# Optimization experiments

Hardware: AMD Instinct MI355X
Metric: run time of the kernel (lower is better)

Reference implementation:

```python
import jax, jax.numpy as jnp
import numpy as np

B, T, C = 2, 2048, 1024
H, D = 16, 64
EPS = 1e-6


def _layernorm(x, gamma, beta):
    # Faithful to the torch module: uses unbiased std (Bessel) and divides by (std + eps).
    mean = x.mean(-1, keepdims=True)
    std = jnp.sqrt(jnp.sum((x - mean) ** 2, axis=-1, keepdims=True) / (x.shape[-1] - 1))
    return gamma * (x - mean) / (std + EPS) + beta


def setup_inputs() -> dict:
    key = jax.random.key(0)
    ks = jax.random.split(key, 9)
    s = lambda fan_in: 1.0 / np.sqrt(fan_in)
    return {
        "x": jax.random.normal(ks[0], (B, T, C), dtype=jnp.float32),
        "qkv_w": jax.random.uniform(ks[1], (3 * C, C), jnp.float32, -s(C), s(C)),
        "proj_w": jax.random.uniform(ks[2], (C, C), jnp.float32, -s(C), s(C)),
        "proj_b": jax.random.uniform(ks[3], (C,), jnp.float32, -s(C), s(C)),
        "l1_w": jax.random.uniform(ks[4], (4 * C, C), jnp.float32, -s(C), s(C)),
        "l1_b": jax.random.uniform(ks[5], (4 * C,), jnp.float32, -s(C), s(C)),
        "l3_w": jax.random.uniform(ks[6], (C, 4 * C), jnp.float32, -s(4 * C), s(4 * C)),
        "l3_b": jax.random.uniform(ks[7], (C,), jnp.float32, -s(4 * C), s(4 * C)),
        "ln1_g": jnp.ones((C,), jnp.float32),
        "ln1_b": jnp.zeros((C,), jnp.float32),
        "ln2_g": jnp.ones((C,), jnp.float32),
        "ln2_b": jnp.zeros((C,), jnp.float32),
    }


def _attention(x, qkv_w, proj_w, proj_b):
    Bx, Tx, Cx = x.shape
    qkv = x @ qkv_w.T                      # [B,T,3C]
    q, k, v = jnp.split(qkv, 3, axis=-1)
    q = q.reshape(Bx, Tx, H, D)
    k = k.reshape(Bx, Tx, H, D)
    v = v.reshape(Bx, Tx, H, D)
    scores = jnp.einsum("bthd,bshd->bhts", q, k) * (D ** -0.5)  # [B,H,T,T]
    causal = jnp.tril(jnp.ones((Tx, Tx), dtype=bool))
    scores = jnp.where(causal, scores, -jnp.inf)
    attn = jax.nn.softmax(scores, axis=-1)
    out = jnp.einsum("bhts,bshd->bthd", attn, v).reshape(Bx, Tx, Cx)
    return out @ proj_w.T + proj_b


def _mlp(x, l1_w, l1_b, l3_w, l3_b):
    h = jax.nn.relu(x @ l1_w.T + l1_b)     # [B,T,4C]
    return h @ l3_w.T + l3_b


def reference(x, qkv_w, proj_w, proj_b, l1_w, l1_b, l3_w, l3_b, ln1_g, ln1_b, ln2_g, ln2_b):
    # Dropout is identity in eval mode.
    x1 = x + _attention(_layernorm(x, ln1_g, ln1_b), qkv_w, proj_w, proj_b)
    x2 = x1 + _mlp(_layernorm(x1, ln2_g, ln2_b), l1_w, l1_b, l3_w, l3_b)
    return x2
```

## Files before the change

kernel.cpp:

```cpp
#include <hip/hip_runtime.h>

typedef unsigned short u16;
typedef short short8 __attribute__((ext_vector_type(8)));
typedef float floatx4 __attribute__((ext_vector_type(4)));

#define TT 2048
#define CC 1024

__device__ __forceinline__ u16 f2bf(float f) {
  unsigned int u = __float_as_uint(f);
  u += 0x7fffu + ((u >> 16) & 1u);
  return (u16)(u >> 16);
}

__device__ __forceinline__ unsigned int pk2bf(float a, float b) {
  unsigned int ua = __float_as_uint(a) + 0x8000u;
  unsigned int ub = __float_as_uint(b) + 0x8000u;
  return (ua >> 16) | (ub & 0xffff0000u);
}

__device__ __forceinline__ void glds16(const u16* g, u16* l) {
  __builtin_amdgcn_global_load_lds((const __attribute__((address_space(1))) void*)g,
                                   (__attribute__((address_space(3))) void*)l, 16, 0, 0);
}

__global__ __launch_bounds__(256) void cvt_all_kernel(const float* __restrict__ w0,
                                                      const float* __restrict__ w1,
                                                      const float* __restrict__ w2,
                                                      const float* __restrict__ w3,
                                                      u16* __restrict__ o0,
                                                      u16* __restrict__ o1,
                                                      u16* __restrict__ o2,
                                                      u16* __restrict__ o3) {
  int blk = blockIdx.x;
  const float* in;
  u16* out;
  int base;
  if (blk < 3072)      { in = w0; out = o0; base = 0; }
  else if (blk < 4096) { in = w1; out = o1; base = 3072; }
  else if (blk < 8192) { in = w2; out = o2; base = 4096; }
  else                 { in = w3; out = o3; base = 8192; }
  int i = (blk - base) * 256 + threadIdx.x;
  float4 v = ((const float4*)in)[i];
  ushort4 o;
  o.x = f2bf(v.x); o.y = f2bf(v.y); o.z = f2bf(v.z); o.w = f2bf(v.w);
  ((ushort4*)out)[i] = o;
}

__global__ __launch_bounds__(256) void ln_kernel(const float* __restrict__ x,
                                                 const float* __restrict__ g,
                                                 const float* __restrict__ b,
                                                 u16* __restrict__ out) {
  int row = blockIdx.x;
  int tid = threadIdx.x;
  const float4* xr = (const float4*)(x + (size_t)row * CC);
  float4 v = xr[tid];
  float s = v.x + v.y + v.z + v.w;
  float sq = v.x * v.x + v.y * v.y + v.z * v.z + v.w * v.w;
#pragma unroll
  for (int off = 1; off < 64; off <<= 1) {
    s += __shfl_xor(s, off);
    sq += __shfl_xor(sq, off);
  }
  __shared__ float ss[4], ssq[4];
  int wave = tid >> 6;
  if ((tid & 63) == 0) { ss[wave] = s; ssq[wave] = sq; }
  __syncthreads();
  s = ss[0] + ss[1] + ss[2] + ss[3];
  sq = ssq[0] + ssq[1] + ssq[2] + ssq[3];
  float mean = s * (1.0f / CC);
  float var = (sq - (float)CC * mean * mean) * (1.0f / (CC - 1));
  float inv = 1.0f / (sqrtf(fmaxf(var, 0.0f)) + 1e-6f);
  float4 gv = ((const float4*)g)[tid];
  float4 bv = ((const float4*)b)[tid];
  ushort4 o;
  o.x = f2bf(gv.x * (v.x - mean) * inv + bv.x);
  o.y = f2bf(gv.y * (v.y - mean) * inv + bv.y);
  o.z = f2bf(gv.z * (v.z - mean) * inv + bv.z);
  o.w = f2bf(gv.w * (v.w - mean) * inv + bv.w);
  ((ushort4*)(out + (size_t)row * CC))[tid] = o;
}

template <int BM, int MODE>
__global__ __launch_bounds__(256) void gemm_bt(const u16* __restrict__ A,
                                               const u16* __restrict__ W,
                                               const float* __restrict__ bias,
                                               const float* __restrict__ resid,
                                               float* __restrict__ outf,
                                               u16* __restrict__ outb,
                                               int M, int N, int K, int lda) {
  constexpr int MI = BM / 32;
  __shared__ u16 a_lds[BM * 64];
  __shared__ u16 b_lds[128 * 64];
  int tid = threadIdx.x;
  int w = tid >> 6, lane = tid & 63;
  int l15 = lane & 15, quad = lane >> 4;
  int wm = (w >> 1) * (MI * 16), wn = (w & 1) * 64;
  int tm = blockIdx.x * BM, tn = blockIdx.y * 128;
  size_t koff = (size_t)blockIdx.z * K;
  floatx4 acc[MI][4];
#pragma unroll
  for (int i = 0; i < MI; i++)
#pragma unroll
    for (int j = 0; j < 4; j++) acc[i][j] = (floatx4){0.f, 0.f, 0.f, 0.f};

  int rsub = lane >> 3;
  int cg = (lane & 7) ^ rsub;
  const u16* Ag = A + (size_t)(tm + w * (BM / 4) + rsub) * lda + koff + cg * 8;
  const u16* Bg = W + (size_t)(tn + w * 32 + rsub) * lda + koff + cg * 8;
  u16* aL = a_lds + w * (BM / 4) * 64;
  u16* bL = b_lds + w * 32 * 64;

  int x = l15 & 7;
  int offA[MI], offB[4];
#pragma unroll
  for (int i = 0; i < MI; i++) offA[i] = (wm + i * 16 + l15) * 64 + ((quad ^ x) * 8);
#pragma unroll
  for (int j = 0; j < 4; j++) offB[j] = (wn + j * 16 + l15) * 64 + ((quad ^ x) * 8);

  for (int k0 = 0; k0 < K; k0 += 64) {
    __syncthreads();
#pragma unroll
    for (int is = 0; is < BM / 32; is++) glds16(Ag + k0 + (size_t)is * 8 * lda, aL + is * 512);
#pragma unroll
    for (int is = 0; is < 4; is++) glds16(Bg + k0 + (size_t)is * 8 * lda, bL + is * 512);
    __syncthreads();
#pragma unroll
    for (int s = 0; s < 2; s++) {
      short8 af[MI], bw[4];
#pragma unroll
      for (int i = 0; i < MI; i++) af[i] = *(const short8*)(a_lds + (offA[i] ^ (s << 5)));
#pragma unroll
      for (int j = 0; j < 4; j++) bw[j] = *(const short8*)(b_lds + (offB[j] ^ (s << 5)));
#pragma unroll
      for (int i = 0; i < MI; i++)
#pragma unroll
        for (int j = 0; j < 4; j++)
          acc[i][j] = __builtin_amdgcn_mfma_f32_16x16x32_bf16(af[i], bw[j], acc[i][j], 0, 0, 0);
    }
  }

  float* po = (MODE == 3) ? outf + (size_t)blockIdx.z * M * N : outf;
#pragma unroll
  for (int i = 0; i < MI; i++) {
    int row0 = tm + wm + i * 16 + quad * 4;
#pragma unroll
    for (int j = 0; j < 4; j++) {
      int col = tn + wn + j * 16 + l15;
      float bb = (MODE == 1 || MODE == 2) ? bias[col] : 0.0f;
#pragma unroll
      for (int r = 0; r < 4; r++) {
        int row = row0 + r;
        float v = acc[i][j][r];
        if (MODE == 0) {
          if (col < 1024) v *= 0.125f;
          outb[(size_t)row * N + col] = f2bf(v);
        } else if (MODE == 1) {
          outf[(size_t)row * N + col] = v + bb + resid[(size_t)row * N + col];
        } else if (MODE == 2) {
          outb[(size_t)row * N + col] = f2bf(fmaxf(v + bb, 0.0f));
        } else {
          po[(size_t)row * N + col] = v;
        }
      }
    }
  }
}

__global__ __launch_bounds__(256) void reduce2_kernel(const float* __restrict__ p,
                                                      const float* __restrict__ bias,
                                                      const float* __restrict__ resid,
                                                      float* __restrict__ out) {
  int i = blockIdx.x * 256 + threadIdx.x;
  float4 a = ((const float4*)p)[i];
  float4 b = ((const float4*)p)[i + 1048576];
  float4 r = ((const float4*)resid)[i];
  float4 bb = ((const float4*)bias)[i & 255];
  float4 o;
  o.x = a.x + b.x + r.x + bb.x;
  o.y = a.y + b.y + r.y + bb.y;
  o.z = a.z + b.z + r.z + bb.z;
  o.w = a.w + b.w + r.w + bb.w;
  ((float4*)out)[i] = o;
}

__global__ __launch_bounds__(256) void flash_kernel(const u16* __restrict__ qkv,
                                                    u16* __restrict__ attn) {
  int bid = blockIdx.x;
  int qt = 31 - (bid >> 5);
  int bh = bid & 31;
  int b = bh >> 4, h = bh & 15;
  int tid = threadIdx.x, w = tid >> 6, lane = tid & 63;
  int l15 = lane & 15, quad = lane >> 4;

  __shared__ u16 k_lds[128 * 64];
  __shared__ u16 vt_lds[64 * 136];
  __shared__ u16 p_lds[4][16 * 136];

  int qbase = qt * 64 + w * 16;
  const u16* qp = qkv + (size_t)(b * TT + qbase + l15) * 3072 + h * 64;
  short8 qf0 = *(const short8*)(qp + quad * 8);
  short8 qf1 = *(const short8*)(qp + 32 + quad * 8);

  float m_i = -3.0e38f, l_i = 0.0f;
  floatx4 accO[4];
#pragma unroll
  for (int jf = 0; jf < 4; jf++) accO[jf] = (floatx4){0.f, 0.f, 0.f, 0.f};

  int rsub = lane >> 3;
  int cg = (lane & 7) ^ rsub;
  const u16* Kg = qkv + (size_t)(b * TT + w * 32 + rsub) * 3072 + 1024 + h * 64 + cg * 8;
  u16* kL = k_lds + w * 32 * 64;
  int s4 = (tid & 31) * 4;
  int dg = (tid >> 5) * 8;
  const u16* Vg = qkv + (size_t)(b * TT + s4) * 3072 + 2048 + h * 64 + dg;

  int x = l15 & 7;
  int kOff[8];
#pragma unroll
  for (int i = 0; i < 8; i++) kOff[i] = (i * 16 + l15) * 64 + ((quad ^ x) * 8);
  int pRd = l15 * 136 + quad * 8;

  int nt = (qt + 2) >> 1;
  for (int kt = 0; kt < nt; kt++) {
    int s0 = kt * 128;
    size_t soff = (size_t)s0 * 3072;
    uint4 R0 = *(const uint4*)(Vg + soff);
    uint4 R1 = *(const uint4*)(Vg + soff + 3072);
    uint4 R2 = *(const uint4*)(Vg + soff + 6144);
    uint4 R3 = *(const uint4*)(Vg + soff + 9216);
    __syncthreads();
#pragma unroll
    for (int is = 0; is < 4; is++) glds16(Kg + soff + (size_t)is * 8 * 3072, kL + is * 512);
    {
      unsigned int a0[4] = {R0.x, R0.y, R0.z, R0.w};
      unsigned int a1[4] = {R1.x, R1.y, R1.z, R1.w};
      unsigned int a2[4] = {R2.x, R2.y, R2.z, R2.w};
      unsigned int a3[4] = {R3.x, R3.y, R3.z, R3.w};
#pragma unroll
      for (int p = 0; p < 4; p++) {
        uint2 ev, od;
        ev.x = (a0[p] & 0xffffu) | (a1[p] << 16);
        ev.y = (a2[p] & 0xffffu) | (a3[p] << 16);
        od.x = (a0[p] >> 16) | (a1[p] & 0xffff0000u);
        od.y = (a2[p] >> 16) | (a3[p] & 0xffff0000u);
        *(uint2*)(vt_lds + (dg + 2 * p) * 136 + s4) = ev;
        *(uint2*)(vt_lds + (dg + 2 * p + 1) * 136 + s4) = od;
      }
    }
    __syncthreads();

    floatx4 st[8];
#pragma unroll
    for (int i = 0; i < 8; i++) st[i] = (floatx4){0.f, 0.f, 0.f, 0.f};
#pragma unroll
    for (int i = 0; i < 8; i++) {
      short8 kf0 = *(const short8*)(k_lds + kOff[i]);
      short8 kf1 = *(const short8*)(k_lds + (kOff[i] ^ 32));
      st[i] = __builtin_amdgcn_mfma_f32_16x16x32_bf16(kf0, qf0, st[i], 0, 0, 0);
      st[i] = __builtin_amdgcn_mfma_f32_16x16x32_bf16(kf1, qf1, st[i], 0, 0, 0);
    }

    if (s0 + 127 > qbase) {
      int mg = qbase + l15;
#pragma unroll
      for (int i = 0; i < 8; i++)
#pragma unroll
        for (int r = 0; r < 4; r++) {
          int s = s0 + i * 16 + quad * 4 + r;
          if (s > mg) st[i][r] = -3.0e38f;
        }
    }

    float mx = st[0][0];
#pragma unroll
    for (int i = 0; i < 8; i++)
#pragma unroll
      for (int r = 0; r < 4; r++) mx = fmaxf(mx, st[i][r]);
    mx = fmaxf(mx, __shfl_xor(mx, 16));
    mx = fmaxf(mx, __shfl_xor(mx, 32));
    float mnew = fmaxf(m_i, mx);
    float alpha = __expf(m_i - mnew);
    float ts = 0.0f;
#pragma unroll
    for (int i = 0; i < 8; i++)
#pragma unroll
      for (int r = 0; r < 4; r++) {
        float p = __expf(st[i][r] - mnew);
        st[i][r] = p;
        ts += p;
      }
    ts += __shfl_xor(ts, 16);
    ts += __shfl_xor(ts, 32);
    l_i = l_i * alpha + ts;
    m_i = mnew;

    float aR[4];
#pragma unroll
    for (int r = 0; r < 4; r++) aR[r] = __shfl(alpha, quad * 4 + r);
#pragma unroll
    for (int jf = 0; jf < 4; jf++)
#pragma unroll
      for (int r = 0; r < 4; r++) accO[jf][r] *= aR[r];

#pragma unroll
    for (int i = 0; i < 8; i++) {
      uint2 pk;
      pk.x = pk2bf(st[i][0], st[i][1]);
      pk.y = pk2bf(st[i][2], st[i][3]);
      *(uint2*)(p_lds[w] + l15 * 136 + i * 16 + quad * 4) = pk;
    }

    short8 pf[4];
#pragma unroll
    for (int c = 0; c < 4; c++) pf[c] = *(const short8*)(p_lds[w] + pRd + c * 32);
#pragma unroll
    for (int jf = 0; jf < 4; jf++) {
      int vOff = (jf * 16 + l15) * 136 + quad * 8;
#pragma unroll
      for (int c = 0; c < 4; c++) {
        short8 vf = *(const short8*)(vt_lds + vOff + c * 32);
        accO[jf] = __builtin_amdgcn_mfma_f32_16x16x32_bf16(pf[c], vf, accO[jf], 0, 0, 0);
      }
    }
  }

  float invl = 1.0f / l_i;
  float iR[4];
#pragma unroll
  for (int r = 0; r < 4; r++) iR[r] = __shfl(invl, quad * 4 + r);
  int orow = b * TT + qbase + quad * 4;
#pragma unroll
  for (int r = 0; r < 4; r++) {
    u16* op = attn + (size_t)(orow + r) * CC + h * 64 + l15;
#pragma unroll
    for (int jf = 0; jf < 4; jf++) op[jf * 16] = f2bf(accO[jf][r] * iR[r]);
  }
}

extern "C" void kernel_launch(void* const* d_in, const int* in_sizes, int n_in,
                              void* d_out, int out_size, void* d_ws, size_t ws_size,
                              hipStream_t stream) {
  const float* x      = (const float*)d_in[0];
  const float* qkv_w  = (const float*)d_in[1];
  const float* proj_w = (const float*)d_in[2];
  const float* proj_b = (const float*)d_in[3];
  const float* l1_w   = (const float*)d_in[4];
  const float* l1_b   = (const float*)d_in[5];
  const float* l3_w   = (const float*)d_in[6];
  const float* l3_b   = (const float*)d_in[7];
  const float* ln1_g  = (const float*)d_in[8];
  const float* ln1_b  = (const float*)d_in[9];
  const float* ln2_g  = (const float*)d_in[10];
  const float* ln2_b  = (const float*)d_in[11];
  float* out = (float*)d_out;
  char* ws = (char*)d_ws;

  u16* w_qkv  = (u16*)(ws + 0);
  u16* w_proj = (u16*)(ws + 6291456);
  u16* w_l1   = (u16*)(ws + 8388608);
  u16* w_l3   = (u16*)(ws + 16777216);
  u16* lnb    = (u16*)(ws + 25165824);
  u16* qkvb   = (u16*)(ws + 33554432);
  u16* attnb  = (u16*)(ws + 58720256);
  float* x1   = (float*)(ws + 67108864);
  u16* hb     = (u16*)(ws + 83886080);
  float* l3p  = (float*)(ws + 33554432);

  cvt_all_kernel<<<12288, 256, 0, stream>>>(qkv_w, proj_w, l1_w, l3_w,
                                            w_qkv, w_proj, w_l1, w_l3);

  ln_kernel<<<4096, 256, 0, stream>>>(x, ln1_g, ln1_b, lnb);
  gemm_bt<128, 0><<<dim3(32, 24), 256, 0, stream>>>(lnb, w_qkv, nullptr, nullptr, nullptr,
                                                    qkvb, 4096, 3072, 1024, 1024);
  flash_kernel<<<1024, 256, 0, stream>>>(qkvb, attnb);
  gemm_bt<64, 1><<<dim3(64, 8), 256, 0, stream>>>(attnb, w_proj, proj_b, x, x1, nullptr,
                                                  4096, 1024, 1024, 1024);
  ln_kernel<<<4096, 256, 0, stream>>>(x1, ln2_g, ln2_b, lnb);
  gemm_bt<128, 2><<<dim3(32, 32), 256, 0, stream>>>(lnb, w_l1, l1_b, nullptr, nullptr, hb,
                                                    4096, 4096, 1024, 1024);
  gemm_bt<64, 3><<<dim3(64, 8, 2), 256, 0, stream>>>(hb, w_l3, nullptr, nullptr, l3p,
                                                     nullptr, 4096, 1024, 2048, 4096);
  reduce2_kernel<<<4096, 256, 0, stream>>>(l3p, l3_b, x1, out);
}
```

Before: 322.3 us.

## Shrink GEMM tiles, use exp2 with folded log2e scale, and byte-perm packing

Templates the GEMM on BN and launches smaller tiles (64x128, 64x64) so every GEMM gets more workgroups and better CU occupancy, at the cost of less operand reuse per tile. Folds log2(e) into the Q scaling (0.125*log2e) so the flash softmax can call the hardware exp2 directly instead of __expf. It also replaces shift/mask bf16 packing and the V transpose shuffles with v_perm byte permutes to cut ALU instructions.

```diff
diff --git a/kernel.cpp b/kernel.cpp
--- a/kernel.cpp
+++ b/kernel.cpp
@@ -6,6 +6,7 @@
 
 #define TT 2048
 #define CC 1024
+#define QSCALE 0.1803368801111244f
 
 __device__ __forceinline__ u16 f2bf(float f) {
   unsigned int u = __float_as_uint(f);
@@ -16,7 +17,7 @@
 __device__ __forceinline__ unsigned int pk2bf(float a, float b) {
   unsigned int ua = __float_as_uint(a) + 0x8000u;
   unsigned int ub = __float_as_uint(b) + 0x8000u;
-  return (ua >> 16) | (ub & 0xffff0000u);
+  return __builtin_amdgcn_perm(ub, ua, 0x07060302u);
 }
 
 __device__ __forceinline__ void glds16(const u16* g, u16* l) {
@@ -81,7 +82,7 @@
   ((ushort4*)(out + (size_t)row * CC))[tid] = o;
 }
 
-template <int BM, int MODE>
+template <int BM, int BN, int MODE>
 __global__ __launch_bounds__(256) void gemm_bt(const u16* __restrict__ A,
                                                const u16* __restrict__ W,
                                                const float* __restrict__ bias,
@@ -90,52 +91,53 @@
                                                u16* __restrict__ outb,
                                                int M, int N, int K, int lda) {
   constexpr int MI = BM / 32;
+  constexpr int NJ = BN / 32;
   __shared__ u16 a_lds[BM * 64];
-  __shared__ u16 b_lds[128 * 64];
+  __shared__ u16 b_lds[BN * 64];
   int tid = threadIdx.x;
   int w = tid >> 6, lane = tid & 63;
   int l15 = lane & 15, quad = lane >> 4;
-  int wm = (w >> 1) * (MI * 16), wn = (w & 1) * 64;
-  int tm = blockIdx.x * BM, tn = blockIdx.y * 128;
+  int wm = (w >> 1) * (MI * 16), wn = (w & 1) * (NJ * 16);
+  int tm = blockIdx.x * BM, tn = blockIdx.y * BN;
   size_t koff = (size_t)blockIdx.z * K;
-  floatx4 acc[MI][4];
+  floatx4 acc[MI][NJ];
 #pragma unroll
   for (int i = 0; i < MI; i++)
 #pragma unroll
-    for (int j = 0; j < 4; j++) acc[i][j] = (floatx4){0.f, 0.f, 0.f, 0.f};
+    for (int j = 0; j < NJ; j++) acc[i][j] = (floatx4){0.f, 0.f, 0.f, 0.f};
 
   int rsub = lane >> 3;
   int cg = (lane & 7) ^ rsub;
   const u16* Ag = A + (size_t)(tm + w * (BM / 4) + rsub) * lda + koff + cg * 8;
-  const u16* Bg = W + (size_t)(tn + w * 32 + rsub) * lda + koff + cg * 8;
+  const u16* Bg = W + (size_t)(tn + w * (BN / 4) + rsub) * lda + koff + cg * 8;
   u16* aL = a_lds + w * (BM / 4) * 64;
-  u16* bL = b_lds + w * 32 * 64;
+  u16* bL = b_lds + w * (BN / 4) * 64;
 
   int x = l15 & 7;
-  int offA[MI], offB[4];
+  int offA[MI], offB[NJ];
 #pragma unroll
   for (int i = 0; i < MI; i++) offA[i] = (wm + i * 16 + l15) * 64 + ((quad ^ x) * 8);
 #pragma unroll
-  for (int j = 0; j < 4; j++) offB[j] = (wn + j * 16 + l15) * 64 + ((quad ^ x) * 8);
+  for (int j = 0; j < NJ; j++) offB[j] = (wn + j * 16 + l15) * 64 + ((quad ^ x) * 8);
 
   for (int k0 = 0; k0 < K; k0 += 64) {
     __syncthreads();
 #pragma unroll
     for (int is = 0; is < BM / 32; is++) glds16(Ag + k0 + (size_t)is * 8 * lda, aL + is * 512);
 #pragma unroll
-    for (int is = 0; is < 4; is++) glds16(Bg + k0 + (size_t)is * 8 * lda, bL + is * 512);
+    for (int is = 0; is < BN / 32; is++) glds16(Bg + k0 + (size_t)is * 8 * lda, bL + is * 512);
     __syncthreads();
 #pragma unroll
     for (int s = 0; s < 2; s++) {
-      short8 af[MI], bw[4];
+      short8 af[MI], bw[NJ];
 #pragma unroll
       for (int i = 0; i < MI; i++) af[i] = *(const short8*)(a_lds + (offA[i] ^ (s << 5)));
 #pragma unroll
-      for (int j = 0; j < 4; j++) bw[j] = *(const short8*)(b_lds + (offB[j] ^ (s << 5)));
+      for (int j = 0; j < NJ; j++) bw[j] = *(const short8*)(b_lds + (offB[j] ^ (s << 5)));
 #pragma unroll
       for (int i = 0; i < MI; i++)
 #pragma unroll
-        for (int j = 0; j < 4; j++)
+        for (int j = 0; j < NJ; j++)
           acc[i][j] = __builtin_amdgcn_mfma_f32_16x16x32_bf16(af[i], bw[j], acc[i][j], 0, 0, 0);
     }
   }
@@ -145,7 +147,7 @@
   for (int i = 0; i < MI; i++) {
     int row0 = tm + wm + i * 16 + quad * 4;
 #pragma unroll
-    for (int j = 0; j < 4; j++) {
+    for (int j = 0; j < NJ; j++) {
       int col = tn + wn + j * 16 + l15;
       float bb = (MODE == 1 || MODE == 2) ? bias[col] : 0.0f;
 #pragma unroll
@@ -153,7 +155,7 @@
         int row = row0 + r;
         float v = acc[i][j][r];
         if (MODE == 0) {
-          if (col < 1024) v *= 0.125f;
+          if (col < 1024) v *= QSCALE;
           outb[(size_t)row * N + col] = f2bf(v);
         } else if (MODE == 1) {
           outf[(size_t)row * N + col] = v + bb + resid[(size_t)row * N + col];
@@ -240,10 +242,10 @@
 #pragma unroll
       for (int p = 0; p < 4; p++) {
         uint2 ev, od;
-        ev.x = (a0[p] & 0xffffu) | (a1[p] << 16);
-        ev.y = (a2[p] & 0xffffu) | (a3[p] << 16);
-        od.x = (a0[p] >> 16) | (a1[p] & 0xffff0000u);
-        od.y = (a2[p] >> 16) | (a3[p] & 0xffff0000u);
+        ev.x = __builtin_amdgcn_perm(a1[p], a0[p], 0x05040100u);
+        ev.y = __builtin_amdgcn_perm(a3[p], a2[p], 0x05040100u);
+        od.x = __builtin_amdgcn_perm(a1[p], a0[p], 0x07060302u);
+        od.y = __builtin_amdgcn_perm(a3[p], a2[p], 0x07060302u);
         *(uint2*)(vt_lds + (dg + 2 * p) * 136 + s4) = ev;
         *(uint2*)(vt_lds + (dg + 2 * p + 1) * 136 + s4) = od;
       }
@@ -280,13 +282,13 @@
     mx = fmaxf(mx, __shfl_xor(mx, 16));
     mx = fmaxf(mx, __shfl_xor(mx, 32));
     float mnew = fmaxf(m_i, mx);
-    float alpha = __expf(m_i - mnew);
+    float alpha = __builtin_amdgcn_exp2f(m_i - mnew);
     float ts = 0.0f;
 #pragma unroll
     for (int i = 0; i < 8; i++)
 #pragma unroll
       for (int r = 0; r < 4; r++) {
-        float p = __expf(st[i][r] - mnew);
+        float p = __builtin_amdgcn_exp2f(st[i][r] - mnew);
         st[i][r] = p;
         ts += p;
       }
@@ -371,15 +373,15 @@
                                             w_qkv, w_proj, w_l1, w_l3);
 
   ln_kernel<<<4096, 256, 0, stream>>>(x, ln1_g, ln1_b, lnb);
-  gemm_bt<128, 0><<<dim3(32, 24), 256, 0, stream>>>(lnb, w_qkv, nullptr, nullptr, nullptr,
-                                                    qkvb, 4096, 3072, 1024, 1024);
+  gemm_bt<64, 128, 0><<<dim3(64, 24), 256, 0, stream>>>(lnb, w_qkv, nullptr, nullptr,
+                                                        nullptr, qkvb, 4096, 3072, 1024, 1024);
   flash_kernel<<<1024, 256, 0, stream>>>(qkvb, attnb);
-  gemm_bt<64, 1><<<dim3(64, 8), 256, 0, stream>>>(attnb, w_proj, proj_b, x, x1, nullptr,
-                                                  4096, 1024, 1024, 1024);
+  gemm_bt<64, 64, 1><<<dim3(64, 16), 256, 0, stream>>>(attnb, w_proj, proj_b, x, x1,
+                                                       nullptr, 4096, 1024, 1024, 1024);
   ln_kernel<<<4096, 256, 0, stream>>>(x1, ln2_g, ln2_b, lnb);
-  gemm_bt<128, 2><<<dim3(32, 32), 256, 0, stream>>>(lnb, w_l1, l1_b, nullptr, nullptr, hb,
-                                                    4096, 4096, 1024, 1024);
-  gemm_bt<64, 3><<<dim3(64, 8, 2), 256, 0, stream>>>(hb, w_l3, nullptr, nullptr, l3p,
-                                                     nullptr, 4096, 1024, 2048, 4096);
+  gemm_bt<64, 128, 2><<<dim3(64, 32), 256, 0, stream>>>(lnb, w_l1, l1_b, nullptr, nullptr,
+                                                        hb, 4096, 4096, 1024, 1024);
+  gemm_bt<64, 64, 3><<<dim3(64, 16, 2), 256, 0, stream>>>(hb, w_l3, nullptr, nullptr, l3p,
+                                                          nullptr, 4096, 1024, 2048, 4096);
   reduce2_kernel<<<4096, 256, 0, stream>>>(l3p, l3_b, x1, out);
 }
```

Measured after the change: 334.2 us. 3.7% more time.
